# Performance work log

Hardware: AMD Instinct MI355X
Metric: run time of the kernel (lower is better)

## Reference

```python
import math
import jax, jax.numpy as jnp
import numpy as np


def setup_inputs() -> dict:
    key = jax.random.key(0)
    bs, n_tok, n_heads, width = 2, 2048, 4, 64
    WIN = 64  # window size == dst_mxlen; every dst row exactly full
    k1, k2, k3 = jax.random.split(key, 3)
    q = jax.random.normal(k1, (bs, n_tok, n_heads, width), jnp.float32)
    k_ = jax.random.normal(k2, (bs, n_tok, n_heads, width), jnp.float32)
    v = jax.random.normal(k3, (bs, n_tok, n_heads, width), jnp.float32)
    d = np.arange(n_tok)
    j = np.arange(WIN)
    dst = np.repeat(d, WIN)                                   # [cl]
    src = ((d[:, None] + j[None, :] - WIN // 2) % n_tok).reshape(-1)
    cnt = np.tile(j, n_tok)
    coo = jnp.asarray(np.stack([dst, src, cnt], axis=1), jnp.int32)  # [cl, 3]
    return {"v": v, "q": q, "k": k_, "coo": coo, "dst_mxlen": WIN, "src_mxlen": WIN}


def reference(v, q, k, coo, dst_mxlen, src_mxlen):
    bs, n_tok, n_heads, width = q.shape
    dst, src, cnt = coo[:, 0], coo[:, 1], coo[:, 2]
    scale = -1.0 / math.sqrt(width)
    # permute to [b, h, n_tok, w], gather along token axis
    qq = q.transpose(0, 2, 1, 3)[:, :, dst, :]   # [b, h, cl, w]
    kk = k.transpose(0, 2, 1, 3)[:, :, src, :]   # [b, h, cl, w]
    ww = jnp.sum(jnp.abs(qq - kk), axis=-1) * scale  # L1 scores [b, h, cl]
    NEG = jnp.asarray(-1e12, q.dtype)
    attn = jnp.full((bs, n_heads, n_tok, dst_mxlen), NEG, q.dtype)
    attn = attn.at[:, :, dst, cnt].set(ww)       # scatter into padded buffer
    attn_sm = jax.nn.softmax(attn, axis=-1)      # [b, h, n_tok, dst_mxlen]
    # gather normalized weights back at coo positions; padded slots would
    # multiply zeros in the original vw buffer, so segment-accumulating only
    # filled entries is exactly the same math as the dense einsum.
    w = attn_sm[:, :, dst, cnt]                  # [b, h, cl]
    vv = v.transpose(0, 2, 1, 3)[:, :, src, :]   # [b, h, cl, w]
    vo = jnp.zeros((bs, n_heads, n_tok, width), q.dtype)
    vo = vo.at[:, :, dst, :].add(w[..., None] * vv)
    return vo.transpose(0, 2, 1, 3)              # [b, n_tok, h, w]
```

## Files before the change

### kernel.cpp

```cpp
#include <hip/hip_runtime.h>

#define BS    2
#define NTOK  2048
#define NH    4
#define W     64
#define HALF  32
#define DTILE 16
#define ND    4
#define NROW  17
#define ROWS  80

template<int CTRL>
__device__ __forceinline__ float fadd_dpp(float x) {
    int y = __builtin_amdgcn_mov_dpp(__float_as_int(x), CTRL, 0xF, 0xF, true);
    return x + __int_as_float(y);
}

__global__ __launch_bounds__(256) void l1attn_win64_v10(
    const float* __restrict__ v,
    const float* __restrict__ q,
    const float* __restrict__ k,
    float* __restrict__ out)
{
    __shared__ alignas(16) float ks[ROWS * W];
    __shared__ alignas(16) float vs[ROWS * W];

    const int tid  = threadIdx.x;
    const int lane = tid & 63;
    const int widx = tid >> 6;

    int bid = blockIdx.x;
    bid = (bid & 7) * 128 + (bid >> 3);

    const int bh = bid >> 7;
    const int d0 = (bid & 127) * DTILE;
    const int h  = bh & (NH - 1);
    const int b  = bh >> 2;
    const int base = b * (NTOK * NH * W) + h * W;

    const int l16 = lane & 15;
    const int r   = lane >> 4;
    const int c0  = l16 * 4;
    const int dw0 = d0 + widx * ND;

    float4 qv[ND];
    #pragma unroll
    for (int dd = 0; dd < ND; ++dd)
        qv[dd] = *(const float4*)(q + base + (dw0 + dd) * (NH * W) + c0);

    #pragma unroll
    for (int i = 0; i < 5; ++i) {
        const int c   = i * 256 + tid;
        const int row = c >> 4;
        const int sub = c & 15;
        const int src = (d0 - HALF + row) & (NTOK - 1);
        const float* gk = k + base + src * (NH * W) + sub * 4;
        const float* gv = v + base + src * (NH * W) + sub * 4;
        char* lk = (char*)ks + (i * 256 + widx * 64) * 16;
        char* lv = (char*)vs + (i * 256 + widx * 64) * 16;
        __builtin_amdgcn_global_load_lds(
            (const __attribute__((address_space(1))) void*)gk,
            (__attribute__((address_space(3))) void*)lk, 16, 0, 0);
        __builtin_amdgcn_global_load_lds(
            (const __attribute__((address_space(1))) void*)gv,
            (__attribute__((address_space(3))) void*)lv, 16, 0, 0);
    }

    float4 acc[ND];
    float  ssum[ND];
    #pragma unroll
    for (int dd = 0; dd < ND; ++dd) {
        acc[dd] = make_float4(0.f, 0.f, 0.f, 0.f);
        ssum[dd] = 0.f;
    }

    const float SC = -0.125f * 1.44269504088896f;
    const int lr0 = widx * ND + r;

    asm volatile("s_waitcnt vmcnt(4)" ::: "memory");
    __builtin_amdgcn_s_barrier();
    __builtin_amdgcn_sched_barrier(0);

    #pragma unroll
    for (int it = 0; it < NROW; ++it) {
        if (it == 9) {
            asm volatile("s_waitcnt vmcnt(0)" ::: "memory");
            __builtin_amdgcn_s_barrier();
            __builtin_amdgcn_sched_barrier(0);
        }
        const int lrow = lr0 + it * 4;
        const float4 kv = *(const float4*)&ks[lrow * W + c0];
        const float4 vv = *(const float4*)&vs[lrow * W + c0];
        #pragma unroll
        for (int dd = 0; dd < ND; ++dd) {
            float t = fabsf(qv[dd].x - kv.x) + fabsf(qv[dd].y - kv.y)
                    + fabsf(qv[dd].z - kv.z) + fabsf(qv[dd].w - kv.w);
            t = fadd_dpp<0xB1>(t);
            t = fadd_dpp<0x4E>(t);
            t = fadd_dpp<0x141>(t);
            t = fadd_dpp<0x128>(t);
            float sc = t * SC;
            if (it == 0)        sc = (r <  dd) ? -1e30f : sc;
            if (it == NROW - 1) sc = (r >= dd) ? -1e30f : sc;
            const float p = __builtin_amdgcn_exp2f(sc);
            ssum[dd] += p;
            acc[dd].x = fmaf(p, vv.x, acc[dd].x);
            acc[dd].y = fmaf(p, vv.y, acc[dd].y);
            acc[dd].z = fmaf(p, vv.z, acc[dd].z);
            acc[dd].w = fmaf(p, vv.w, acc[dd].w);
        }
    }

    #pragma unroll
    for (int dd = 0; dd < ND; ++dd) {
        ssum[dd] += __shfl_xor(ssum[dd], 16);
        ssum[dd] += __shfl_xor(ssum[dd], 32);
        acc[dd].x += __shfl_xor(acc[dd].x, 16);
        acc[dd].y += __shfl_xor(acc[dd].y, 16);
        acc[dd].z += __shfl_xor(acc[dd].z, 16);
        acc[dd].w += __shfl_xor(acc[dd].w, 16);
        acc[dd].x += __shfl_xor(acc[dd].x, 32);
        acc[dd].y += __shfl_xor(acc[dd].y, 32);
        acc[dd].z += __shfl_xor(acc[dd].z, 32);
        acc[dd].w += __shfl_xor(acc[dd].w, 32);
    }
    if (r == 0) {
        #pragma unroll
        for (int dd = 0; dd < ND; ++dd) {
            const float inv = 1.0f / ssum[dd];
            *(float4*)(out + base + (dw0 + dd) * (NH * W) + c0) =
                make_float4(acc[dd].x * inv, acc[dd].y * inv,
                            acc[dd].z * inv, acc[dd].w * inv);
        }
    }
}

extern "C" void kernel_launch(void* const* d_in, const int* in_sizes, int n_in,
                              void* d_out, int out_size, void* d_ws, size_t ws_size,
                              hipStream_t stream) {
    const float* v = (const float*)d_in[0];
    const float* q = (const float*)d_in[1];
    const float* k = (const float*)d_in[2];
    float* out = (float*)d_out;

    const int blocks = (BS * NH * NTOK) / DTILE;
    hipLaunchKernelGGL(l1attn_win64_v10, dim3(blocks), dim3(256), 0, stream,
                       v, q, k, out);
}
```

Before: 16.06 us.

## Process two destination tiles per block to reuse K/V halo rows

Each block now handles 32 destination rows as two 16-row sub-tiles, staging 96 K/V rows into LDS instead of 80 per 16 rows. This cuts redundant global loads of the overlapping window halo and halves the block count. The second sub-tile waits on the remaining loads through a second barrier. The cost is fewer blocks (512) for latency hiding, more LDS per block, and more live registers for the doubled q vectors.

Result: slower. 17.71 us (+10.2%).

```diff
diff --git a/kernel.cpp b/kernel.cpp
--- a/kernel.cpp
+++ b/kernel.cpp
@@ -6,9 +6,10 @@
 #define W     64
 #define HALF  32
 #define DTILE 16
+#define NTILE 2
 #define ND    4
 #define NROW  17
-#define ROWS  80
+#define ROWS  96
 
 template<int CTRL>
 __device__ __forceinline__ float fadd_dpp(float x) {
@@ -16,7 +17,7 @@
     return x + __int_as_float(y);
 }
 
-__global__ __launch_bounds__(256) void l1attn_win64_v10(
+__global__ __launch_bounds__(256) void l1attn_win64_v12(
     const float* __restrict__ v,
     const float* __restrict__ q,
     const float* __restrict__ k,
@@ -30,10 +31,10 @@
     const int widx = tid >> 6;
 
     int bid = blockIdx.x;
-    bid = (bid & 7) * 128 + (bid >> 3);
+    bid = (bid & 7) * 64 + (bid >> 3);
 
-    const int bh = bid >> 7;
-    const int d0 = (bid & 127) * DTILE;
+    const int bh = bid >> 6;
+    const int d0 = (bid & 63) * (DTILE * NTILE);
     const int h  = bh & (NH - 1);
     const int b  = bh >> 2;
     const int base = b * (NTOK * NH * W) + h * W;
@@ -41,12 +42,14 @@
     const int l16 = lane & 15;
     const int r   = lane >> 4;
     const int c0  = l16 * 4;
-    const int dw0 = d0 + widx * ND;
 
-    float4 qv[ND];
+    float4 qv[NTILE][ND];
     #pragma unroll
-    for (int dd = 0; dd < ND; ++dd)
-        qv[dd] = *(const float4*)(q + base + (dw0 + dd) * (NH * W) + c0);
+    for (int t = 0; t < NTILE; ++t)
+        #pragma unroll
+        for (int dd = 0; dd < ND; ++dd)
+            qv[t][dd] = *(const float4*)
+                (q + base + (d0 + t * DTILE + widx * ND + dd) * (NH * W) + c0);
 
     #pragma unroll
     for (int i = 0; i < 5; ++i) {
@@ -54,83 +57,105 @@
         const int row = c >> 4;
         const int sub = c & 15;
         const int src = (d0 - HALF + row) & (NTOK - 1);
-        const float* gk = k + base + src * (NH * W) + sub * 4;
-        const float* gv = v + base + src * (NH * W) + sub * 4;
-        char* lk = (char*)ks + (i * 256 + widx * 64) * 16;
-        char* lv = (char*)vs + (i * 256 + widx * 64) * 16;
         __builtin_amdgcn_global_load_lds(
-            (const __attribute__((address_space(1))) void*)gk,
-            (__attribute__((address_space(3))) void*)lk, 16, 0, 0);
+            (const __attribute__((address_space(1))) void*)
+                (k + base + src * (NH * W) + sub * 4),
+            (__attribute__((address_space(3))) void*)
+                ((char*)ks + (i * 256 + widx * 64) * 16), 16, 0, 0);
         __builtin_amdgcn_global_load_lds(
-            (const __attribute__((address_space(1))) void*)gv,
-            (__attribute__((address_space(3))) void*)lv, 16, 0, 0);
+            (const __attribute__((address_space(1))) void*)
+                (v + base + src * (NH * W) + sub * 4),
+            (__attribute__((address_space(3))) void*)
+                ((char*)vs + (i * 256 + widx * 64) * 16), 16, 0, 0);
     }
-
-    float4 acc[ND];
-    float  ssum[ND];
-    #pragma unroll
-    for (int dd = 0; dd < ND; ++dd) {
-        acc[dd] = make_float4(0.f, 0.f, 0.f, 0.f);
-        ssum[dd] = 0.f;
+    {
+        const int c   = 1280 + tid;
+        const int row = c >> 4;
+        const int sub = c & 15;
+        const int src = (d0 - HALF + row) & (NTOK - 1);
+        __builtin_amdgcn_global_load_lds(
+            (const __attribute__((address_space(1))) void*)
+                (k + base + src * (NH * W) + sub * 4),
+            (__attribute__((address_space(3))) void*)
+                ((char*)ks + (1280 + widx * 64) * 16), 16, 0, 0);
+        __builtin_amdgcn_global_load_lds(
+            (const __attribute__((address_space(1))) void*)
+                (v + base + src * (NH * W) + sub * 4),
+            (__attribute__((address_space(3))) void*)
+                ((char*)vs + (1280 + widx * 64) * 16), 16, 0, 0);
     }
 
     const float SC = -0.125f * 1.44269504088896f;
-    const int lr0 = widx * ND + r;
 
-    asm volatile("s_waitcnt vmcnt(4)" ::: "memory");
+    asm volatile("s_waitcnt vmcnt(2)" ::: "memory");
     __builtin_amdgcn_s_barrier();
     __builtin_amdgcn_sched_barrier(0);
 
     #pragma unroll
-    for (int it = 0; it < NROW; ++it) {
-        if (it == 9) {
+    for (int t = 0; t < NTILE; ++t) {
+        if (t == 1) {
             asm volatile("s_waitcnt vmcnt(0)" ::: "memory");
             __builtin_amdgcn_s_barrier();
             __builtin_amdgcn_sched_barrier(0);
         }
-        const int lrow = lr0 + it * 4;
-        const float4 kv = *(const float4*)&ks[lrow * W + c0];
-        const float4 vv = *(const float4*)&vs[lrow * W + c0];
+
+        float4 acc[ND];
+        float  ssum[ND];
         #pragma unroll
         for (int dd = 0; dd < ND; ++dd) {
-            float t = fabsf(qv[dd].x - kv.x) + fabsf(qv[dd].y - kv.y)
-                    + fabsf(qv[dd].z - kv.z) + fabsf(qv[dd].w - kv.w);
-            t = fadd_dpp<0xB1>(t);
-            t = fadd_dpp<0x4E>(t);
-            t = fadd_dpp<0x141>(t);
-            t = fadd_dpp<0x128>(t);
-            float sc = t * SC;
-            if (it == 0)        sc = (r <  dd) ? -1e30f : sc;
-            if (it == NROW - 1) sc = (r >= dd) ? -1e30f : sc;
-            const float p = __builtin_amdgcn_exp2f(sc);
-            ssum[dd] += p;
-            acc[dd].x = fmaf(p, vv.x, acc[dd].x);
-            acc[dd].y = fmaf(p, vv.y, acc[dd].y);
-            acc[dd].z = fmaf(p, vv.z, acc[dd].z);
-            acc[dd].w = fmaf(p, vv.w, acc[dd].w);
+            acc[dd] = make_float4(0.f, 0.f, 0.f, 0.f);
+            ssum[dd] = 0.f;
         }
-    }
 
-    #pragma unroll
-    for (int dd = 0; dd < ND; ++dd) {
-        ssum[dd] += __shfl_xor(ssum[dd], 16);
-        ssum[dd] += __shfl_xor(ssum[dd], 32);
-        acc[dd].x += __shfl_xor(acc[dd].x, 16);
-        acc[dd].y += __shfl_xor(acc[dd].y, 16);
-        acc[dd].z += __shfl_xor(acc[dd].z, 16);
-        acc[dd].w += __shfl_xor(acc[dd].w, 16);
-        acc[dd].x += __shfl_xor(acc[dd].x, 32);
-        acc[dd].y += __shfl_xor(acc[dd].y, 32);
-        acc[dd].z += __shfl_xor(acc[dd].z, 32);
-        acc[dd].w += __shfl_xor(acc[dd].w, 32);
-    }
-    if (r == 0) {
+        const int lr0 = t * DTILE + widx * ND + r;
+
+        #pragma unroll
+        for (int it = 0; it < NROW; ++it) {
+            const int lrow = lr0 + it * 4;
+            const float4 kv = *(const float4*)&ks[lrow * W + c0];
+            const float4 vv = *(const float4*)&vs[lrow * W + c0];
+            #pragma unroll
+            for (int dd = 0; dd < ND; ++dd) {
+                float tt = fabsf(qv[t][dd].x - kv.x) + fabsf(qv[t][dd].y - kv.y)
+                         + fabsf(qv[t][dd].z - kv.z) + fabsf(qv[t][dd].w - kv.w);
+                tt = fadd_dpp<0xB1>(tt);
+                tt = fadd_dpp<0x4E>(tt);
+                tt = fadd_dpp<0x141>(tt);
+                tt = fadd_dpp<0x128>(tt);
+                float sc = tt * SC;
+                if (it == 0)        sc = (r <  dd) ? -1e30f : sc;
+                if (it == NROW - 1) sc = (r >= dd) ? -1e30f : sc;
+                const float p = __builtin_amdgcn_exp2f(sc);
+                ssum[dd] += p;
+                acc[dd].x = fmaf(p, vv.x, acc[dd].x);
+                acc[dd].y = fmaf(p, vv.y, acc[dd].y);
+                acc[dd].z = fmaf(p, vv.z, acc[dd].z);
+                acc[dd].w = fmaf(p, vv.w, acc[dd].w);
+            }
+        }
+
         #pragma unroll
         for (int dd = 0; dd < ND; ++dd) {
-            const float inv = 1.0f / ssum[dd];
-            *(float4*)(out + base + (dw0 + dd) * (NH * W) + c0) =
-                make_float4(acc[dd].x * inv, acc[dd].y * inv,
-                            acc[dd].z * inv, acc[dd].w * inv);
+            ssum[dd] += __shfl_xor(ssum[dd], 16);
+            ssum[dd] += __shfl_xor(ssum[dd], 32);
+            acc[dd].x += __shfl_xor(acc[dd].x, 16);
+            acc[dd].y += __shfl_xor(acc[dd].y, 16);
+            acc[dd].z += __shfl_xor(acc[dd].z, 16);
+            acc[dd].w += __shfl_xor(acc[dd].w, 16);
+            acc[dd].x += __shfl_xor(acc[dd].x, 32);
+            acc[dd].y += __shfl_xor(acc[dd].y, 32);
+            acc[dd].z += __shfl_xor(acc[dd].z, 32);
+            acc[dd].w += __shfl_xor(acc[dd].w, 32);
+        }
+        if (r == 0) {
+            #pragma unroll
+            for (int dd = 0; dd < ND; ++dd) {
+                const float inv = 1.0f / ssum[dd];
+                *(float4*)(out + base +
+                           (d0 + t * DTILE + widx * ND + dd) * (NH * W) + c0) =
+                    make_float4(acc[dd].x * inv, acc[dd].y * inv,
+                                acc[dd].z * inv, acc[dd].w * inv);
+            }
         }
     }
 }
@@ -143,7 +168,7 @@
     const float* k = (const float*)d_in[2];
     float* out = (float*)d_out;
 
-    const int blocks = (BS * NH * NTOK) / DTILE;
-    hipLaunchKernelGGL(l1attn_win64_v10, dim3(blocks), dim3(256), 0, stream,
+    const int blocks = (BS * NH * NTOK) / (DTILE * NTILE);
+    hipLaunchKernelGGL(l1attn_win64_v12, dim3(blocks), dim3(256), 0, stream,
                        v, q, k, out);
 }
```
